# Kernel optimization log

Measured on AMD Instinct MI355X. Metric: run time of the kernel, lower is better.

Reference implementation:

```python
import jax, jax.numpy as jnp
import numpy as np

D_MODEL = 1024
N_HEADS = 16
RANK = 128
N_COMPRESS = 16
N_KNOWLEDGE = 32768
KNOWLEDGE_K = 8
B, S = 4, 1024
EPS = 1e-5


def setup_inputs() -> dict:
    key = jax.random.key(0)
    ks = jax.random.split(key, 16)
    inp = {
        'x': jax.random.normal(ks[0], (B, S, D_MODEL), jnp.float32),
        'mask': jnp.tril(jnp.ones((S, S), bool))[None, None],  # causal [1,1,S,S]
        'compress_neurons': jax.random.normal(ks[1], (N_COMPRESS, D_MODEL, RANK), jnp.float32) / np.sqrt(D_MODEL),
        'knowledge_K': jax.random.normal(ks[2], (N_KNOWLEDGE, RANK), jnp.float32) * 0.02,
        'knowledge_V': jax.random.normal(ks[3], (N_KNOWLEDGE, D_MODEL), jnp.float32) * 0.02,
        'router_Q': jax.random.normal(ks[4], (D_MODEL, N_COMPRESS), jnp.float32) * 0.02,
        'router_K': jax.random.normal(ks[5], (D_MODEL, N_COMPRESS), jnp.float32) * 0.02,
        'router_V': jax.random.normal(ks[6], (D_MODEL, N_COMPRESS), jnp.float32) * 0.02,
        'router_M': jax.random.normal(ks[7], (D_MODEL, N_COMPRESS), jnp.float32) * 0.02,
        'W_Q': jax.random.normal(ks[8], (RANK, D_MODEL), jnp.float32) / np.sqrt(RANK),
        'W_K': jax.random.normal(ks[9], (RANK, D_MODEL), jnp.float32) / np.sqrt(RANK),
        'W_V': jax.random.normal(ks[10], (RANK, D_MODEL), jnp.float32) / np.sqrt(RANK),
        'W_O': jax.random.normal(ks[11], (D_MODEL, D_MODEL), jnp.float32) / np.sqrt(D_MODEL),
        'ln1_g': jnp.ones((D_MODEL,), jnp.float32),
        'ln1_b': jnp.zeros((D_MODEL,), jnp.float32),
        'ln2_g': jnp.ones((D_MODEL,), jnp.float32),
        'ln2_b': jnp.zeros((D_MODEL,), jnp.float32),
    }
    return inp


def _layernorm(x, g, b):
    mu = x.mean(-1, keepdims=True)
    var = ((x - mu) ** 2).mean(-1, keepdims=True)
    return (x - mu) * jax.lax.rsqrt(var + EPS) * g + b


def _compress(x, router_W, neurons):
    # x: [B,S,D]; router_W: [D,N]; neurons: [N,D,R]
    weights = jax.nn.softmax(x @ router_W, axis=-1)               # [B,S,N]
    all_proj = jnp.einsum('bsd,ndr->bsnr', x, neurons)            # [B,S,N,R]
    return jnp.einsum('bsnr,bsn->bsr', all_proj, weights)         # [B,S,R]


def reference(x, mask, compress_neurons, knowledge_K, knowledge_V,
              router_Q, router_K, router_V, router_M,
              W_Q, W_K, W_V, W_O, ln1_g, ln1_b, ln2_g, ln2_b):
    d_head = D_MODEL // N_HEADS
    h = _layernorm(x, ln1_g, ln1_b)
    # soft-routed low-rank compression for Q/K/V
    hQ = _compress(h, router_Q, compress_neurons)
    hK = _compress(h, router_K, compress_neurons)
    hV = _compress(h, router_V, compress_neurons)
    Q = (hQ @ W_Q).reshape(B, S, N_HEADS, d_head).transpose(0, 2, 1, 3)
    K = (hK @ W_K).reshape(B, S, N_HEADS, d_head).transpose(0, 2, 1, 3)
    V = (hV @ W_V).reshape(B, S, N_HEADS, d_head).transpose(0, 2, 1, 3)
    scores = jnp.einsum('bhqd,bhkd->bhqk', Q, K) / np.sqrt(d_head)
    scores = jnp.where(mask, scores, -jnp.inf)
    attn = jax.nn.softmax(scores, axis=-1)
    attn_out = jnp.einsum('bhqk,bhkd->bhqd', attn, V)
    attn_out = attn_out.transpose(0, 2, 1, 3).reshape(B, S, D_MODEL)
    x = x + attn_out @ W_O
    # knowledge memory
    h2 = _layernorm(x, ln2_g, ln2_b)
    Qm = _compress(h2, router_M, compress_neurons)                # [B,S,R]
    kscores = Qm @ knowledge_K.T / np.sqrt(RANK)                  # [B,S,NK]
    topk_scores, topk_idx = jax.lax.top_k(kscores, KNOWLEDGE_K)
    kweights = jax.nn.softmax(topk_scores, axis=-1)               # [B,S,k]
    selected_V = knowledge_V[topk_idx]                            # [B,S,k,D]
    mem_out = jnp.einsum('bskd,bsk->bsd', selected_V, kweights)
    return x + mem_out
```

## Files before the change

### kernel.cpp

```cpp
#include <hip/hip_runtime.h>
#include <math.h>

#define DM     1024
#define RANK   128
#define NCMP   16
#define NKNOW  32768
#define TOPK   8
#define NROWS  4096
#define NEG_BIG -3.0e38f
#define TK_SPLIT 32
#define TK_KEYS (NKNOW / TK_SPLIT)

typedef __attribute__((ext_vector_type(8))) short s8v;
typedef __attribute__((ext_vector_type(4))) float f4v;

__device__ __forceinline__ unsigned short f2bf(float f) {
  union { float fl; unsigned u; } v; v.fl = f;
  return (unsigned short)((v.u + 0x7FFFu + ((v.u >> 16) & 1u)) >> 16);
}
__device__ __forceinline__ float bf2f(unsigned short u) {
  return __uint_as_float((unsigned)u << 16);
}
__device__ __forceinline__ f4v mfma16(s8v a, s8v b, f4v c) {
  return __builtin_amdgcn_mfma_f32_16x16x32_bf16(a, b, c, 0, 0, 0);
}
__device__ __forceinline__ unsigned umed3(unsigned a, unsigned b, unsigned c) {
  unsigned d;
  asm("v_med3_u32 %0, %1, %2, %3" : "=v"(d) : "v"(a), "v"(b), "v"(c));
  return d;
}
__device__ __forceinline__ void gload16(const unsigned short* g, unsigned short* l) {
  __builtin_amdgcn_global_load_lds(
      (const __attribute__((address_space(1))) unsigned int*)(g),
      (__attribute__((address_space(3))) unsigned int*)(l), 16, 0, 0);
}

__global__ __launch_bounds__(256) void ln_kernel(const float* __restrict__ x,
                                                 const float* __restrict__ g,
                                                 const float* __restrict__ b,
                                                 unsigned short* __restrict__ obf) {
  __shared__ float red1[4], red2[4];
  const int row = blockIdx.x, t = threadIdx.x;
  const float4 v = reinterpret_cast<const float4*>(x + (size_t)row * DM)[t];
  float s = v.x + v.y + v.z + v.w;
#pragma unroll
  for (int m = 1; m <= 32; m <<= 1) s += __shfl_xor(s, m);
  if ((t & 63) == 0) red1[t >> 6] = s;
  __syncthreads();
  const float mu = (red1[0] + red1[1] + red1[2] + red1[3]) * (1.0f / DM);
  const float dx = v.x - mu, dy = v.y - mu, dz = v.z - mu, dw = v.w - mu;
  float ss = dx * dx + dy * dy + dz * dz + dw * dw;
#pragma unroll
  for (int m = 1; m <= 32; m <<= 1) ss += __shfl_xor(ss, m);
  if ((t & 63) == 0) red2[t >> 6] = ss;
  __syncthreads();
  const float var = (red2[0] + red2[1] + red2[2] + red2[3]) * (1.0f / DM);
  const float inv = rsqrtf(var + 1e-5f);
  const float4 g4 = reinterpret_cast<const float4*>(g)[t];
  const float4 b4 = reinterpret_cast<const float4*>(b)[t];
  ushort4 u = make_ushort4(f2bf(dx * inv * g4.x + b4.x), f2bf(dy * inv * g4.y + b4.y),
                           f2bf(dz * inv * g4.z + b4.z), f2bf(dw * inv * g4.w + b4.w));
  reinterpret_cast<ushort4*>(obf + (size_t)row * DM)[t] = u;
}

__device__ __forceinline__ void tcvt_body(const float* __restrict__ in,
                                          unsigned short* __restrict__ out,
                                          int K, int N, int bx, int by, int bz, int t) {
  __shared__ float ld[32][33];
  const int k0 = by * 32, n0 = bx * 32;
  const float* ib = in + (size_t)bz * K * N;
  unsigned short* ob = out + (size_t)bz * K * N;
  const int kl = t >> 3, nl = (t & 7) * 4;
  const float4 v = *reinterpret_cast<const float4*>(&ib[(size_t)(k0 + kl) * N + n0 + nl]);
  ld[kl][nl] = v.x; ld[kl][nl + 1] = v.y; ld[kl][nl + 2] = v.z; ld[kl][nl + 3] = v.w;
  __syncthreads();
  const int nw = t >> 3, kw = (t & 7) * 4;
  ushort4 o = make_ushort4(f2bf(ld[kw][nw]), f2bf(ld[kw + 1][nw]),
                           f2bf(ld[kw + 2][nw]), f2bf(ld[kw + 3][nw]));
  *reinterpret_cast<ushort4*>(&ob[(size_t)(n0 + nw) * K + k0 + kw]) = o;
}

__global__ __launch_bounds__(256) void prep_kernel(const float* __restrict__ kK,
                                                   unsigned short* __restrict__ kKb,
                                                   const float* __restrict__ neur,
                                                   unsigned short* __restrict__ neurT,
                                                   const float* __restrict__ WQ,
                                                   const float* __restrict__ WK,
                                                   const float* __restrict__ WV,
                                                   unsigned short* __restrict__ WQKVt,
                                                   const float* __restrict__ WO,
                                                   unsigned short* __restrict__ WOt) {
  const int bid = blockIdx.x, t = threadIdx.x;
  if (bid < 2048) {
    const int i = bid * 256 + t;
    const float4 a = reinterpret_cast<const float4*>(kK)[2 * i];
    const float4 b = reinterpret_cast<const float4*>(kK)[2 * i + 1];
    reinterpret_cast<ushort4*>(kKb)[2 * i] =
        make_ushort4(f2bf(a.x), f2bf(a.y), f2bf(a.z), f2bf(a.w));
    reinterpret_cast<ushort4*>(kKb)[2 * i + 1] =
        make_ushort4(f2bf(b.x), f2bf(b.y), f2bf(b.z), f2bf(b.w));
  } else if (bid < 4096) {
    const int lb = bid - 2048;
    tcvt_body(neur, neurT, DM, RANK, lb & 3, (lb >> 2) & 31, lb >> 7, t);
  } else if (bid < 4224) {
    const int lb = bid - 4096;
    tcvt_body(WQ, WQKVt, RANK, DM, lb & 31, lb >> 5, 0, t);
  } else if (bid < 4352) {
    const int lb = bid - 4224;
    tcvt_body(WK, WQKVt + (size_t)DM * RANK, RANK, DM, lb & 31, lb >> 5, 0, t);
  } else if (bid < 4480) {
    const int lb = bid - 4352;
    tcvt_body(WV, WQKVt + (size_t)2 * DM * RANK, RANK, DM, lb & 31, lb >> 5, 0, t);
  } else {
    const int lb = bid - 4480;
    tcvt_body(WO, WOt, DM, DM, lb & 31, lb >> 5, 0, t);
  }
}

__global__ __launch_bounds__(256) void vtr_kernel(const unsigned short* __restrict__ V,
                                                  unsigned short* __restrict__ Vt) {
  __shared__ unsigned short ld[32][40];
  const int bh = blockIdx.z, b = bh >> 4, hh = bh & 15;
  const int s0 = blockIdx.x * 32, d0 = blockIdx.y * 32;
  const int t = threadIdx.x;
  const int r = t >> 3, c = (t & 7) * 4;
  *reinterpret_cast<ushort4*>(&ld[r][c]) =
      *reinterpret_cast<const ushort4*>(&V[(size_t)(b * 1024 + s0 + r) * DM + hh * 64 + d0 + c]);
  __syncthreads();
  ushort4 o;
  o.x = ld[c + 0][r]; o.y = ld[c + 1][r]; o.z = ld[c + 2][r]; o.w = ld[c + 3][r];
  *reinterpret_cast<ushort4*>(&Vt[((size_t)bh * 64 + d0 + r) * 1024 + s0 + c]) = o;
}

__global__ __launch_bounds__(256) void router3_kernel(const unsigned short* __restrict__ h,
                                                      const float* __restrict__ R0,
                                                      const float* __restrict__ R1,
                                                      const float* __restrict__ R2,
                                                      float* __restrict__ w0,
                                                      float* __restrict__ w1,
                                                      float* __restrict__ w2) {
  __shared__ float hs[DM];
  __shared__ float red[3][16][17];
  const int row = blockIdx.x, t = threadIdx.x;
  {
    const ushort4 u = reinterpret_cast<const ushort4*>(h + (size_t)row * DM)[t];
    hs[t * 4 + 0] = bf2f(u.x); hs[t * 4 + 1] = bf2f(u.y);
    hs[t * 4 + 2] = bf2f(u.z); hs[t * 4 + 3] = bf2f(u.w);
  }
  __syncthreads();
  const int o = t & 15, seg = t >> 4;
  float a0 = 0.f, a1 = 0.f, a2 = 0.f;
  for (int d = seg * 64; d < seg * 64 + 64; ++d) {
    const float hv = hs[d];
    a0 += hv * R0[d * NCMP + o];
    a1 += hv * R1[d * NCMP + o];
    a2 += hv * R2[d * NCMP + o];
  }
  red[0][seg][o] = a0; red[1][seg][o] = a1; red[2][seg][o] = a2;
  __syncthreads();
  if (t < 48) {
    const int g = t >> 4, oo = t & 15;
    float dot = 0.f;
#pragma unroll
    for (int s = 0; s < 16; ++s) dot += red[g][s][oo];
    float m = dot;
#pragma unroll
    for (int msk = 1; msk < 16; msk <<= 1) m = fmaxf(m, __shfl_xor(m, msk));
    const float e = __expf(dot - m);
    float ssum = e;
#pragma unroll
    for (int msk = 1; msk < 16; msk <<= 1) ssum += __shfl_xor(ssum, msk);
    float* wp = (g == 0) ? w0 : (g == 1) ? w1 : w2;
    wp[(size_t)row * NCMP + oo] = e / ssum;
  }
}

__global__ __launch_bounds__(256) void router_kernel(const unsigned short* __restrict__ h,
                                                     const float* __restrict__ R,
                                                     float* __restrict__ w) {
  __shared__ float hs[DM];
  __shared__ float red[16][17];
  const int row = blockIdx.x, t = threadIdx.x;
  {
    const ushort4 u = reinterpret_cast<const ushort4*>(h + (size_t)row * DM)[t];
    hs[t * 4 + 0] = bf2f(u.x); hs[t * 4 + 1] = bf2f(u.y);
    hs[t * 4 + 2] = bf2f(u.z); hs[t * 4 + 3] = bf2f(u.w);
  }
  __syncthreads();
  const int o = t & 15, seg = t >> 4;
  float acc = 0.f;
  for (int d = seg * 64; d < seg * 64 + 64; ++d) acc += hs[d] * R[d * NCMP + o];
  red[seg][o] = acc;
  __syncthreads();
  if (t < 16) {
    float dot = 0.f;
#pragma unroll
    for (int s = 0; s < 16; ++s) dot += red[s][t];
    float m = dot;
#pragma unroll
    for (int msk = 1; msk < 16; msk <<= 1) m = fmaxf(m, __shfl_xor(m, msk));
    const float e = __expf(dot - m);
    float ssum = e;
#pragma unroll
    for (int msk = 1; msk < 16; msk <<= 1) ssum += __shfl_xor(ssum, msk);
    w[(size_t)row * NCMP + t] = e / ssum;
  }
}

template <bool OUT_BF16, bool RES>
__global__ __launch_bounds__(256) void mfma_nt(const unsigned short* __restrict__ A,
                                               const unsigned short* __restrict__ B,
                                               float* __restrict__ Cf,
                                               unsigned short* __restrict__ Cb,
                                               const float* __restrict__ res,
                                               int M, int N, int K, int bshift) {
  __shared__ unsigned short As[2][128 * 64];
  __shared__ unsigned short Bs[2][128 * 64];
  const int t = threadIdx.x;
  const int lane = t & 63, w = t >> 6;
  const int wm = w >> 1, wn = w & 1;
  const int bm = blockIdx.y, bn = blockIdx.x;
  const int l15 = lane & 15, l4 = lane >> 4;
  f4v acc[4][4] = {};
  const int srow = w * 32 + (lane >> 3);
  const int scol = ((lane & 7) ^ (lane >> 3)) * 8;
  const unsigned short* ga = A + (size_t)(bm * 128 + srow) * K + scol;
  const unsigned short* gb = B + (size_t)(bm >> bshift) * ((size_t)N * K) +
                             (size_t)(bn * 128 + srow) * K + scol;
  const int NITER = K >> 6;
#pragma unroll
  for (int j = 0; j < 4; ++j) {
    gload16(ga + (size_t)j * 8 * K, &As[0][w * 2048 + j * 512]);
    gload16(gb + (size_t)j * 8 * K, &Bs[0][w * 2048 + j * 512]);
  }
  __syncthreads();
  for (int it = 0; it < NITER; ++it) {
    const int cur = it & 1;
    if (it + 1 < NITER) {
      const int k0 = (it + 1) * 64;
      unsigned short* const nA = &As[cur ^ 1][w * 2048];
      unsigned short* const nB = &Bs[cur ^ 1][w * 2048];
#pragma unroll
      for (int j = 0; j < 4; ++j) {
        gload16(ga + (size_t)j * 8 * K + k0, nA + j * 512);
        gload16(gb + (size_t)j * 8 * K + k0, nB + j * 512);
      }
    }
#pragma unroll
    for (int ks = 0; ks < 2; ++ks) {
      s8v af[4], bf[4];
      const int sc = (ks * 32 + l4 * 8) ^ ((l15 & 7) * 8);
#pragma unroll
      for (int i = 0; i < 4; ++i) {
        af[i] = *reinterpret_cast<const s8v*>(&As[cur][(wm * 64 + i * 16 + l15) * 64 + sc]);
        bf[i] = *reinterpret_cast<const s8v*>(&Bs[cur][(wn * 64 + i * 16 + l15) * 64 + sc]);
      }
#pragma unroll
      for (int i = 0; i < 4; ++i)
#pragma unroll
        for (int j = 0; j < 4; ++j) acc[i][j] = mfma16(af[i], bf[j], acc[i][j]);
    }
    __syncthreads();
  }
#pragma unroll
  for (int i = 0; i < 4; ++i) {
#pragma unroll
    for (int j = 0; j < 4; ++j) {
#pragma unroll
      for (int r = 0; r < 4; ++r) {
        const int row = bm * 128 + wm * 64 + i * 16 + l4 * 4 + r;
        const int col = bn * 128 + wn * 64 + j * 16 + l15;
        float v = acc[i][j][r];
        if constexpr (RES) v += res[(size_t)row * N + col];
        if constexpr (OUT_BF16) Cb[(size_t)row * N + col] = f2bf(v);
        else Cf[(size_t)row * N + col] = v;
      }
    }
  }
}

__global__ __launch_bounds__(128) void wsum_kernel(const unsigned short* __restrict__ ap,
                                                   const float* __restrict__ w0,
                                                   const float* __restrict__ w1,
                                                   const float* __restrict__ w2,
                                                   unsigned short* __restrict__ o0,
                                                   unsigned short* __restrict__ o1,
                                                   unsigned short* __restrict__ o2,
                                                   float scale) {
  const int row = blockIdx.x, r = threadIdx.x;
  float wa[16], wb[16], wc[16];
#pragma unroll
  for (int n = 0; n < 16; ++n) wa[n] = w0[(size_t)row * NCMP + n];
  if (w1) {
#pragma unroll
    for (int n = 0; n < 16; ++n) wb[n] = w1[(size_t)row * NCMP + n];
  }
  if (w2) {
#pragma unroll
    for (int n = 0; n < 16; ++n) wc[n] = w2[(size_t)row * NCMP + n];
  }
  float a0 = 0.f, a1 = 0.f, a2 = 0.f;
  const unsigned short* apr = ap + (size_t)row * (NCMP * RANK) + r;
#pragma unroll
  for (int n = 0; n < 16; ++n) {
    const float v = bf2f(apr[n * RANK]);
    a0 += v * wa[n];
    if (w1) a1 += v * wb[n];
    if (w2) a2 += v * wc[n];
  }
  o0[(size_t)row * RANK + r] = f2bf(a0 * scale);
  if (o1) o1[(size_t)row * RANK + r] = f2bf(a1 * scale);
  if (o2) o2[(size_t)row * RANK + r] = f2bf(a2 * scale);
}

__global__ __launch_bounds__(256) void flash_kernel(const unsigned short* __restrict__ Q,
                                                    const unsigned short* __restrict__ K,
                                                    const unsigned short* __restrict__ Vt,
                                                    unsigned short* __restrict__ O) {
  __shared__ unsigned short Qs[64 * 72], Ks[64 * 72], Vs[64 * 72], Ps[64 * 72];
  const int bh = blockIdx.x, qt = blockIdx.y;
  const int b = bh >> 4, hh = bh & 15;
  const int base = b * 1024, q0 = qt * 64, col = hh * 64;
  const int t = threadIdx.x;
  const int lane = t & 63, w = t >> 6;
  const int l15 = lane & 15, l4 = lane >> 4;
  const int sr = t >> 2, soff = (t & 3) * 16;
  const unsigned short* Vh = Vt + (size_t)bh * 64 * 1024;
  *reinterpret_cast<s8v*>(&Qs[sr * 72 + soff]) =
      *reinterpret_cast<const s8v*>(&Q[(size_t)(base + q0 + sr) * DM + col + soff]);
  *reinterpret_cast<s8v*>(&Qs[sr * 72 + soff + 8]) =
      *reinterpret_cast<const s8v*>(&Q[(size_t)(base + q0 + sr) * DM + col + soff + 8]);
  *reinterpret_cast<s8v*>(&Ks[sr * 72 + soff]) =
      *reinterpret_cast<const s8v*>(&K[(size_t)(base + sr) * DM + col + soff]);
  *reinterpret_cast<s8v*>(&Ks[sr * 72 + soff + 8]) =
      *reinterpret_cast<const s8v*>(&K[(size_t)(base + sr) * DM + col + soff + 8]);
  *reinterpret_cast<s8v*>(&Vs[sr * 72 + soff]) =
      *reinterpret_cast<const s8v*>(&Vh[(size_t)sr * 1024 + soff]);
  *reinterpret_cast<s8v*>(&Vs[sr * 72 + soff + 8]) =
      *reinterpret_cast<const s8v*>(&Vh[(size_t)sr * 1024 + soff + 8]);
  float m_r[4], l_r[4];
  f4v o[4] = {};
#pragma unroll
  for (int r = 0; r < 4; ++r) { m_r[r] = NEG_BIG; l_r[r] = 0.f; }
  __syncthreads();
  for (int kt = 0; kt <= qt; ++kt) {
    const int k0 = kt * 64;
    const bool pre = kt < qt;
    s8v stk0, stk1, stv0, stv1;
    if (pre) {
      const int kn = k0 + 64;
      stk0 = *reinterpret_cast<const s8v*>(&K[(size_t)(base + kn + sr) * DM + col + soff]);
      stk1 = *reinterpret_cast<const s8v*>(&K[(size_t)(base + kn + sr) * DM + col + soff + 8]);
      stv0 = *reinterpret_cast<const s8v*>(&Vh[(size_t)sr * 1024 + kn + soff]);
      stv1 = *reinterpret_cast<const s8v*>(&Vh[(size_t)sr * 1024 + kn + soff + 8]);
    }
    f4v s[4] = {};
#pragma unroll
    for (int ks = 0; ks < 2; ++ks) {
      s8v a = *reinterpret_cast<const s8v*>(&Qs[(w * 16 + l15) * 72 + ks * 32 + l4 * 8]);
#pragma unroll
      for (int nj = 0; nj < 4; ++nj) {
        s8v bb = *reinterpret_cast<const s8v*>(&Ks[(nj * 16 + l15) * 72 + ks * 32 + l4 * 8]);
        s[nj] = mfma16(a, bb, s[nj]);
      }
    }
#pragma unroll
    for (int r = 0; r < 4; ++r) {
      const int grow = q0 + w * 16 + l4 * 4 + r;
      float sv[4];
#pragma unroll
      for (int nj = 0; nj < 4; ++nj) {
        const float xx = s[nj][r] * 0.125f;
        const int gcol = k0 + nj * 16 + l15;
        sv[nj] = (gcol <= grow) ? xx : NEG_BIG;
      }
      float mt = fmaxf(fmaxf(sv[0], sv[1]), fmaxf(sv[2], sv[3]));
#pragma unroll
      for (int msk = 1; msk < 16; msk <<= 1) mt = fmaxf(mt, __shfl_xor(mt, msk));
      const float mn = fmaxf(m_r[r], mt);
      const float sc = __expf(m_r[r] - mn);
      m_r[r] = mn;
      float rs = 0.f, pv[4];
#pragma unroll
      for (int nj = 0; nj < 4; ++nj) { pv[nj] = __expf(sv[nj] - mn); rs += pv[nj]; }
#pragma unroll
      for (int msk = 1; msk < 16; msk <<= 1) rs += __shfl_xor(rs, msk);
      l_r[r] = l_r[r] * sc + rs;
#pragma unroll
      for (int nd = 0; nd < 4; ++nd) o[nd][r] *= sc;
#pragma unroll
      for (int nj = 0; nj < 4; ++nj)
        Ps[(w * 16 + l4 * 4 + r) * 72 + nj * 16 + l15] = f2bf(pv[nj]);
    }
#pragma unroll
    for (int ks = 0; ks < 2; ++ks) {
      s8v pa = *reinterpret_cast<const s8v*>(&Ps[(w * 16 + l15) * 72 + ks * 32 + l4 * 8]);
#pragma unroll
      for (int nd = 0; nd < 4; ++nd) {
        s8v vb = *reinterpret_cast<const s8v*>(&Vs[(nd * 16 + l15) * 72 + ks * 32 + l4 * 8]);
        o[nd] = mfma16(pa, vb, o[nd]);
      }
    }
    __syncthreads();
    if (pre) {
      *reinterpret_cast<s8v*>(&Ks[sr * 72 + soff]) = stk0;
      *reinterpret_cast<s8v*>(&Ks[sr * 72 + soff + 8]) = stk1;
      *reinterpret_cast<s8v*>(&Vs[sr * 72 + soff]) = stv0;
      *reinterpret_cast<s8v*>(&Vs[sr * 72 + soff + 8]) = stv1;
    }
    __syncthreads();
  }
#pragma unroll
  for (int nd = 0; nd < 4; ++nd)
#pragma unroll
    for (int r = 0; r < 4; ++r) {
      const int grow = base + q0 + w * 16 + l4 * 4 + r;
      O[(size_t)grow * DM + col + nd * 16 + l15] = f2bf(o[nd][r] / l_r[r]);
    }
}

__global__ __launch_bounds__(256) void topk_kernel(const unsigned short* __restrict__ Qm,
                                                   const unsigned short* __restrict__ kK,
                                                   float* __restrict__ tks,
                                                   int* __restrict__ tki) {
  __shared__ __align__(16) char arena[16384];
  unsigned short* const Kt0 = (unsigned short*)arena;
  unsigned short* const Kt1 = (unsigned short*)(arena + 8192);
  const int id = blockIdx.x;
  const int sp = (id & 7) * 4 + ((id >> 3) & 3);
  const int rb = id >> 5;
  const int r0 = rb * 64, kb0 = sp * TK_KEYS;
  const int t = threadIdx.x;
  const int lane = t & 63, w = t >> 6;
  const int l15 = lane & 15, l4 = lane >> 4;
  s8v qf[4];
#pragma unroll
  for (int ks = 0; ks < 4; ++ks)
    qf[ks] = *reinterpret_cast<const s8v*>(
        &Qm[(size_t)(r0 + w * 16 + l15) * RANK + ks * 32 + l4 * 8]);
  unsigned bs0 = 0u, bs1 = 0u, bs2 = 0u, bs3 = 0u, bs4 = 0u, bs5 = 0u, bs6 = 0u, bs7 = 0u;
  const int s0i = 2 * w, s1i = 2 * w + 1;
  const unsigned short* g0 = kK + (size_t)(kb0 + (s0i >> 2) * 16 + l15) * RANK + (s0i & 3) * 32 + l4 * 8;
  const unsigned short* g1 = kK + (size_t)(kb0 + (s1i >> 2) * 16 + l15) * RANK + (s1i & 3) * 32 + l4 * 8;
  const int NCH = TK_KEYS / 32;
  gload16(g0, Kt0 + s0i * 512);
  gload16(g1, Kt0 + s1i * 512);
  __syncthreads();
  for (int ch = 0; ch < NCH; ++ch) {
    const unsigned short* const bufc = (ch & 1) ? Kt1 : Kt0;
    unsigned short* const bufn = (ch & 1) ? Kt0 : Kt1;
    if (ch + 1 < NCH) {
      const size_t off = (size_t)(ch + 1) * 32 * RANK;
      gload16(g0 + off, bufn + s0i * 512);
      gload16(g1 + off, bufn + s1i * 512);
    }
    f4v acc[2];
    acc[0] = f4v{4.f, 4.f, 4.f, 4.f};
    acc[1] = f4v{4.f, 4.f, 4.f, 4.f};
#pragma unroll
    for (int kt = 0; kt < 2; ++kt) {
#pragma unroll
      for (int ks = 0; ks < 4; ++ks) {
        s8v a = *reinterpret_cast<const s8v*>(&bufc[(kt * 4 + ks) * 512 + lane * 8]);
        acc[kt] = mfma16(a, qf[ks], acc[kt]);
      }
    }
    const unsigned invbase = 2047u - (unsigned)(ch * 32 + l4 * 4);
#pragma unroll
    for (int kt = 0; kt < 2; ++kt) {
#pragma unroll
      for (int r = 0; r < 4; ++r) {
        const unsigned u = __float_as_uint(acc[kt][r]);
        const unsigned pk = (u & 0xFFFFF800u) | (invbase - (unsigned)(kt * 16 + r));
        bs7 = umed3(bs6, pk, bs7);
        bs6 = umed3(bs5, pk, bs6);
        bs5 = umed3(bs4, pk, bs5);
        bs4 = umed3(bs3, pk, bs4);
        bs3 = umed3(bs2, pk, bs3);
        bs2 = umed3(bs1, pk, bs2);
        bs1 = umed3(bs0, pk, bs1);
        bs0 = max(bs0, pk);
      }
    }
    __syncthreads();
  }
  unsigned* const M = (unsigned*)arena;
  const int row = w * 16 + l15;
  {
    unsigned* mp = M + row * 33 + l4 * 8;
    mp[0] = bs0; mp[1] = bs1; mp[2] = bs2; mp[3] = bs3;
    mp[4] = bs4; mp[5] = bs5; mp[6] = bs6; mp[7] = bs7;
  }
  __syncthreads();
  if (t < 64) {
    const unsigned* mr = M + t * 33;
    int h0 = 0, h1 = 0, h2 = 0, h3 = 0;
    const size_t oo = ((size_t)sp * NROWS + r0 + t) * TOPK;
    for (int k = 0; k < TOPK; ++k) {
      const unsigned c0 = (h0 < 8) ? mr[0 + h0] : 0u;
      const unsigned c1 = (h1 < 8) ? mr[8 + h1] : 0u;
      const unsigned c2 = (h2 < 8) ? mr[16 + h2] : 0u;
      const unsigned c3 = (h3 < 8) ? mr[24 + h3] : 0u;
      const unsigned m01 = (c0 >= c1) ? c0 : c1; const int l01 = (c0 >= c1) ? 0 : 1;
      const unsigned m23 = (c2 >= c3) ? c2 : c3; const int l23 = (c2 >= c3) ? 2 : 3;
      const unsigned bst = (m01 >= m23) ? m01 : m23;
      const int bl = (m01 >= m23) ? l01 : l23;
      tks[oo + k] = __uint_as_float(bst & 0xFFFFF800u) - 4.0f;
      tki[oo + k] = kb0 + 2047 - (int)(bst & 0x7FFu);
      h0 += (bl == 0); h1 += (bl == 1); h2 += (bl == 2); h3 += (bl == 3);
    }
  }
}

__global__ __launch_bounds__(256) void gather_kernel(const float* __restrict__ tks,
                                                     const int* __restrict__ tki,
                                                     const float* __restrict__ kV,
                                                     float* __restrict__ out) {
  __shared__ float ls[TK_SPLIT * TOPK];
  __shared__ int li[TK_SPLIT * TOPK];
  __shared__ float selv[TOPK];
  __shared__ int seli[TOPK];
  __shared__ float wsel[TOPK];
  const int row = blockIdx.x, t = threadIdx.x;
  if (t < TK_SPLIT * TOPK) {
    const int l = t >> 3, k = t & 7;
    ls[t] = tks[((size_t)l * NROWS + row) * TOPK + k];
    li[t] = tki[((size_t)l * NROWS + row) * TOPK + k];
  }
  __syncthreads();
  if (t < TK_SPLIT * TOPK) {
    const float v = ls[t];
    const int myid = li[t];
    int rank = 0;
    for (int j = 0; j < TK_SPLIT * TOPK; ++j) {
      const float u = ls[j];
      rank += (u > v) || (u == v && li[j] < myid);
    }
    if (rank < TOPK) { selv[rank] = v; seli[rank] = myid; }
  }
  __syncthreads();
  if (t == 0) {
    const float m = selv[0];
    float sum = 0.f, e[TOPK];
#pragma unroll
    for (int k = 0; k < TOPK; ++k) { e[k] = __expf(selv[k] - m); sum += e[k]; }
    const float inv = 1.f / sum;
#pragma unroll
    for (int k = 0; k < TOPK; ++k) wsel[k] = e[k] * inv;
  }
  __syncthreads();
  float4 accv = reinterpret_cast<float4*>(out + (size_t)row * DM)[t];
#pragma unroll
  for (int k = 0; k < TOPK; ++k) {
    const float4 v4 = reinterpret_cast<const float4*>(kV + (size_t)seli[k] * DM)[t];
    const float wk = wsel[k];
    accv.x += wk * v4.x; accv.y += wk * v4.y; accv.z += wk * v4.z; accv.w += wk * v4.w;
  }
  reinterpret_cast<float4*>(out + (size_t)row * DM)[t] = accv;
}

extern "C" void kernel_launch(void* const* d_in, const int* in_sizes, int n_in,
                              void* d_out, int out_size, void* d_ws, size_t ws_size,
                              hipStream_t stream) {
  (void)in_sizes; (void)n_in; (void)out_size; (void)ws_size;
  const float* x    = (const float*)d_in[0];
  const float* neur = (const float*)d_in[2];
  const float* kK   = (const float*)d_in[3];
  const float* kV   = (const float*)d_in[4];
  const float* rQ   = (const float*)d_in[5];
  const float* rK   = (const float*)d_in[6];
  const float* rV   = (const float*)d_in[7];
  const float* rM   = (const float*)d_in[8];
  const float* WQ   = (const float*)d_in[9];
  const float* WK   = (const float*)d_in[10];
  const float* WV   = (const float*)d_in[11];
  const float* WO   = (const float*)d_in[12];
  const float* g1   = (const float*)d_in[13];
  const float* b1   = (const float*)d_in[14];
  const float* g2   = (const float*)d_in[15];
  const float* b2   = (const float*)d_in[16];
  float* out = (float*)d_out;

  char* base = (char*)d_ws;
  auto alloc = [&](size_t bytes) { char* r = base; base += (bytes + 255) & ~(size_t)255; return r; };
  unsigned short* hbf   = (unsigned short*)alloc((size_t)NROWS * DM * 2);
  unsigned short* apb   = (unsigned short*)alloc((size_t)3 * NROWS * DM * 2);
  unsigned short* neurT = (unsigned short*)alloc((size_t)NCMP * RANK * DM * 2);
  unsigned short* WQKVt = (unsigned short*)alloc((size_t)3 * DM * RANK * 2);
  unsigned short* WOt   = (unsigned short*)alloc((size_t)DM * DM * 2);
  unsigned short* kKb   = (unsigned short*)alloc((size_t)NKNOW * RANK * 2);
  unsigned short* hQKVb = (unsigned short*)alloc((size_t)3 * NROWS * RANK * 2);
  unsigned short* Qmb   = (unsigned short*)alloc((size_t)NROWS * RANK * 2);
  unsigned short* Vtb   = (unsigned short*)alloc((size_t)NROWS * DM * 2);
  float* wQw = (float*)alloc((size_t)NROWS * NCMP * 4);
  float* wKw = (float*)alloc((size_t)NROWS * NCMP * 4);
  float* wVw = (float*)alloc((size_t)NROWS * NCMP * 4);
  float* wMw = (float*)alloc((size_t)NROWS * NCMP * 4);
  float* tks = (float*)alloc((size_t)TK_SPLIT * NROWS * TOPK * 4);
  int*   tki = (int*)alloc((size_t)TK_SPLIT * NROWS * TOPK * 4);
  unsigned short* Qb = apb;
  unsigned short* Kb = Qb + (size_t)NROWS * DM;
  unsigned short* Vb = Kb + (size_t)NROWS * DM;
  unsigned short* attnb = hbf;
  unsigned short* hQb = hQKVb;
  unsigned short* hKb = hQKVb + (size_t)NROWS * RANK;
  unsigned short* hVb = hQKVb + (size_t)2 * NROWS * RANK;

  prep_kernel<<<5504, 256, 0, stream>>>(kK, kKb, neur, neurT, WQ, WK, WV, WQKVt, WO, WOt);

  ln_kernel<<<NROWS, 256, 0, stream>>>(x, g1, b1, hbf);
  mfma_nt<true, false><<<dim3(16, 32), 256, 0, stream>>>(hbf, neurT, nullptr, apb, nullptr,
                                                         NROWS, NCMP * RANK, DM, 30);
  router3_kernel<<<NROWS, 256, 0, stream>>>(hbf, rQ, rK, rV, wQw, wKw, wVw);
  wsum_kernel<<<NROWS, 128, 0, stream>>>(apb, wQw, wKw, wVw, hQb, hKb, hVb, 1.0f);
  mfma_nt<true, false><<<dim3(8, 96), 256, 0, stream>>>(hQKVb, WQKVt, nullptr, Qb, nullptr,
                                                        3 * NROWS, DM, RANK, 5);
  vtr_kernel<<<dim3(32, 2, 64), 256, 0, stream>>>(Vb, Vtb);
  flash_kernel<<<dim3(64, 16), 256, 0, stream>>>(Qb, Kb, Vtb, attnb);
  mfma_nt<false, true><<<dim3(8, 32), 256, 0, stream>>>(attnb, WOt, out, nullptr, x,
                                                        NROWS, DM, DM, 30);

  ln_kernel<<<NROWS, 256, 0, stream>>>(out, g2, b2, hbf);
  mfma_nt<true, false><<<dim3(16, 32), 256, 0, stream>>>(hbf, neurT, nullptr, apb, nullptr,
                                                         NROWS, NCMP * RANK, DM, 30);
  router_kernel<<<NROWS, 256, 0, stream>>>(hbf, rM, wMw);
  wsum_kernel<<<NROWS, 128, 0, stream>>>(apb, wMw, nullptr, nullptr, Qmb, nullptr, nullptr,
                                         0.08838834764831845f );
  topk_kernel<<<2048, 256, 0, stream>>>(Qmb, kKb, tks, tki);
  gather_kernel<<<NROWS, 256, 0, stream>>>(tks, tki, kV, out);
}
```

Before: 335.1 us.

## Use vmcnt waits with single barrier and 4-stage LDS ring in topk and GEMM

The GEMM loop swaps the __syncthreads around its global-to-LDS loads for explicit s_waitcnt vmcnt counters plus raw s_barrier. A prefetch can now be issued before waiting on the current tile. The topk kernel moves from a 2-buffer to a 4-buffer LDS ring, which removes the trailing barrier per chunk, and unrolls the chunk loop by four through a macro. This cuts barrier stalls and overlaps loads with MFMA and the top-k insertion chain, at the cost of doubled LDS in topk and reliance on hand-counted vmcnt correctness.

```diff
diff --git a/kernel.cpp b/kernel.cpp
--- a/kernel.cpp
+++ b/kernel.cpp
@@ -34,6 +34,8 @@
       (const __attribute__((address_space(1))) unsigned int*)(g),
       (__attribute__((address_space(3))) unsigned int*)(l), 16, 0, 0);
 }
+#define VMCNT(n) asm volatile("s_waitcnt vmcnt(" #n ")" ::: "memory")
+#define BAR() __builtin_amdgcn_s_barrier()
 
 __global__ __launch_bounds__(256) void ln_kernel(const float* __restrict__ x,
                                                  const float* __restrict__ g,
@@ -233,7 +235,6 @@
     gload16(ga + (size_t)j * 8 * K, &As[0][w * 2048 + j * 512]);
     gload16(gb + (size_t)j * 8 * K, &Bs[0][w * 2048 + j * 512]);
   }
-  __syncthreads();
   for (int it = 0; it < NITER; ++it) {
     const int cur = it & 1;
     if (it + 1 < NITER) {
@@ -245,7 +246,11 @@
         gload16(ga + (size_t)j * 8 * K + k0, nA + j * 512);
         gload16(gb + (size_t)j * 8 * K + k0, nB + j * 512);
       }
-    }
+      VMCNT(8);
+    } else {
+      VMCNT(0);
+    }
+    BAR();
 #pragma unroll
     for (int ks = 0; ks < 2; ++ks) {
       s8v af[4], bf[4];
@@ -260,7 +265,7 @@
 #pragma unroll
         for (int j = 0; j < 4; ++j) acc[i][j] = mfma16(af[i], bf[j], acc[i][j]);
     }
-    __syncthreads();
+    BAR();
   }
 #pragma unroll
   for (int i = 0; i < 4; ++i) {
@@ -423,9 +428,11 @@
                                                    const unsigned short* __restrict__ kK,
                                                    float* __restrict__ tks,
                                                    int* __restrict__ tki) {
-  __shared__ __align__(16) char arena[16384];
-  unsigned short* const Kt0 = (unsigned short*)arena;
-  unsigned short* const Kt1 = (unsigned short*)(arena + 8192);
+  __shared__ __align__(16) char arena[32768];
+  unsigned short* const K0 = (unsigned short*)arena;
+  unsigned short* const K1 = (unsigned short*)(arena + 8192);
+  unsigned short* const K2 = (unsigned short*)(arena + 16384);
+  unsigned short* const K3 = (unsigned short*)(arena + 24576);
   const int id = blockIdx.x;
   const int sp = (id & 7) * 4 + ((id >> 3) & 3);
   const int rb = id >> 5;
@@ -442,48 +449,58 @@
   const int s0i = 2 * w, s1i = 2 * w + 1;
   const unsigned short* g0 = kK + (size_t)(kb0 + (s0i >> 2) * 16 + l15) * RANK + (s0i & 3) * 32 + l4 * 8;
   const unsigned short* g1 = kK + (size_t)(kb0 + (s1i >> 2) * 16 + l15) * RANK + (s1i & 3) * 32 + l4 * 8;
-  const int NCH = TK_KEYS / 32;
-  gload16(g0, Kt0 + s0i * 512);
-  gload16(g1, Kt0 + s1i * 512);
-  __syncthreads();
-  for (int ch = 0; ch < NCH; ++ch) {
-    const unsigned short* const bufc = (ch & 1) ? Kt1 : Kt0;
-    unsigned short* const bufn = (ch & 1) ? Kt0 : Kt1;
-    if (ch + 1 < NCH) {
-      const size_t off = (size_t)(ch + 1) * 32 * RANK;
-      gload16(g0 + off, bufn + s0i * 512);
-      gload16(g1 + off, bufn + s1i * 512);
-    }
-    f4v acc[2];
-    acc[0] = f4v{4.f, 4.f, 4.f, 4.f};
-    acc[1] = f4v{4.f, 4.f, 4.f, 4.f};
-#pragma unroll
-    for (int kt = 0; kt < 2; ++kt) {
-#pragma unroll
-      for (int ks = 0; ks < 4; ++ks) {
-        s8v a = *reinterpret_cast<const s8v*>(&bufc[(kt * 4 + ks) * 512 + lane * 8]);
-        acc[kt] = mfma16(a, qf[ks], acc[kt]);
-      }
-    }
-    const unsigned invbase = 2047u - (unsigned)(ch * 32 + l4 * 4);
-#pragma unroll
-    for (int kt = 0; kt < 2; ++kt) {
-#pragma unroll
-      for (int r = 0; r < 4; ++r) {
-        const unsigned u = __float_as_uint(acc[kt][r]);
-        const unsigned pk = (u & 0xFFFFF800u) | (invbase - (unsigned)(kt * 16 + r));
-        bs7 = umed3(bs6, pk, bs7);
-        bs6 = umed3(bs5, pk, bs6);
-        bs5 = umed3(bs4, pk, bs5);
-        bs4 = umed3(bs3, pk, bs4);
-        bs3 = umed3(bs2, pk, bs3);
-        bs2 = umed3(bs1, pk, bs2);
-        bs1 = umed3(bs0, pk, bs1);
-        bs0 = max(bs0, pk);
-      }
-    }
-    __syncthreads();
-  }
+  gload16(g0, K0 + s0i * 512);
+  gload16(g1, K0 + s1i * 512);
+
+#define TK_STEP(BC, BN, CH)                                                        \
+  {                                                                                \
+    if ((CH) + 1 < 32) {                                                           \
+      const size_t off_ = (size_t)((CH) + 1) * 32 * RANK;                          \
+      gload16(g0 + off_, (BN) + s0i * 512);                                        \
+      gload16(g1 + off_, (BN) + s1i * 512);                                        \
+      VMCNT(2);                                                                    \
+    } else {                                                                       \
+      VMCNT(0);                                                                    \
+    }                                                                              \
+    BAR();                                                                         \
+    f4v a0_ = f4v{4.f, 4.f, 4.f, 4.f};                                             \
+    f4v a1_ = f4v{4.f, 4.f, 4.f, 4.f};                                             \
+    _Pragma("unroll")                                                              \
+    for (int ks_ = 0; ks_ < 4; ++ks_) {                                            \
+      a0_ = mfma16(*reinterpret_cast<const s8v*>(&(BC)[ks_ * 512 + lane * 8]),     \
+                   qf[ks_], a0_);                                                  \
+      a1_ = mfma16(*reinterpret_cast<const s8v*>(&(BC)[(4 + ks_) * 512 + lane * 8]),\
+                   qf[ks_], a1_);                                                  \
+    }                                                                              \
+    const unsigned ivb_ = 2047u - (unsigned)((CH) * 32 + l4 * 4);                  \
+    _Pragma("unroll")                                                              \
+    for (int r_ = 0; r_ < 4; ++r_) {                                               \
+      const unsigned u_ = __float_as_uint(a0_[r_]);                                \
+      const unsigned pk_ = (u_ & 0xFFFFF800u) | (ivb_ - (unsigned)r_);             \
+      bs7 = umed3(bs6, pk_, bs7); bs6 = umed3(bs5, pk_, bs6);                      \
+      bs5 = umed3(bs4, pk_, bs5); bs4 = umed3(bs3, pk_, bs4);                      \
+      bs3 = umed3(bs2, pk_, bs3); bs2 = umed3(bs1, pk_, bs2);                      \
+      bs1 = umed3(bs0, pk_, bs1); bs0 = max(bs0, pk_);                             \
+    }                                                                              \
+    _Pragma("unroll")                                                              \
+    for (int r_ = 0; r_ < 4; ++r_) {                                               \
+      const unsigned u_ = __float_as_uint(a1_[r_]);                                \
+      const unsigned pk_ = (u_ & 0xFFFFF800u) | (ivb_ - (unsigned)(16 + r_));      \
+      bs7 = umed3(bs6, pk_, bs7); bs6 = umed3(bs5, pk_, bs6);                      \
+      bs5 = umed3(bs4, pk_, bs5); bs4 = umed3(bs3, pk_, bs4);                      \
+      bs3 = umed3(bs2, pk_, bs3); bs2 = umed3(bs1, pk_, bs2);                      \
+      bs1 = umed3(bs0, pk_, bs1); bs0 = max(bs0, pk_);                             \
+    }                                                                              \
+  }
+
+  for (int c4 = 0; c4 < 32; c4 += 4) {
+    TK_STEP(K0, K1, c4 + 0);
+    TK_STEP(K1, K2, c4 + 1);
+    TK_STEP(K2, K3, c4 + 2);
+    TK_STEP(K3, K0, c4 + 3);
+  }
+#undef TK_STEP
+
   unsigned* const M = (unsigned*)arena;
   const int row = w * 16 + l15;
   {
```

New measurement: 311.3 us. 1.08x faster.
